# Kernel tuning notes

Measured on AMD Instinct MI355X. Metric: run time of the kernel, lower is better.

## Reference

```python
import math
import jax, jax.numpy as jnp
import numpy as np

B, C, DM, H = 4, 2048, 128, 8  # batch, after_reduced_cnn_size (seq), d_model, heads
DPH = DM // H                  # 16
K = 7                          # causal conv kernel size


def _causal_conv1d(x, w, b):
    # x: (B, C, L); w: (C_out, C_in, K); left-pad by K-1 -> causal, 'same' length
    xp = jnp.pad(x, ((0, 0), (0, 0), (w.shape[-1] - 1, 0)))
    y = jax.lax.conv_general_dilated(xp, w, (1,), 'VALID',
                                     dimension_numbers=('NCH', 'OIH', 'NCH'))
    return y + b[None, :, None]


def _split_heads(x):
    # (B, S, H*DPH) layout after view: (B, C, DM) -> (B, H, C, DPH)
    return x.reshape(x.shape[0], -1, H, DPH).transpose(0, 2, 1, 3)


def setup_inputs() -> dict:
    rng = jax.random.key(0)
    ks = jax.random.split(rng, 9)
    conv_scale = 1.0 / math.sqrt(C * K)
    lin_scale = 1.0 / math.sqrt(DM)
    return {
        'query': jax.random.normal(ks[0], (B, C, DM), dtype=jnp.float32),
        'key': jax.random.normal(ks[1], (B, C, DM), dtype=jnp.float32),
        'value': jax.random.normal(ks[2], (B, C, DM), dtype=jnp.float32),
        'conv_k_w': jax.random.normal(ks[3], (C, C, K), dtype=jnp.float32) * conv_scale,
        'conv_k_b': jnp.zeros((C,), dtype=jnp.float32),
        'conv_v_w': jax.random.normal(ks[4], (C, C, K), dtype=jnp.float32) * conv_scale,
        'conv_v_b': jnp.zeros((C,), dtype=jnp.float32),
        'lin_w': jax.random.normal(ks[5], (DM, DM), dtype=jnp.float32) * lin_scale,
        'lin_b': jnp.zeros((DM,), dtype=jnp.float32),
    }


def reference(query, key, value, conv_k_w, conv_k_b, conv_v_w, conv_v_b, lin_w, lin_b):
    # query used as-is; key/value pass through causal convs (convs[1], convs[2])
    q = _split_heads(query)                                   # (B,H,C,DPH)
    k = _split_heads(_causal_conv1d(key, conv_k_w, conv_k_b))  # (B,H,C,DPH)
    v = _split_heads(_causal_conv1d(value, conv_v_w, conv_v_b))
    scores = jnp.einsum('bhqd,bhkd->bhqk', q, k) / math.sqrt(DPH)
    p = jax.nn.softmax(scores, axis=-1)                       # (B,H,C,C)
    x = jnp.einsum('bhqk,bhkd->bhqd', p, v)                   # dropout p=0 => same as x_raw
    x = x.transpose(0, 2, 1, 3).reshape(x.shape[0], -1, H * DPH)
    return x @ lin_w.T + lin_b
```

## Files before the change

### kernel.cpp

```cpp
#include <hip/hip_runtime.h>
#include <cstdint>
#include <cstddef>

#define B_   4
#define C_   2048
#define DM_  128
#define H_   8
#define KK_  14336
#define N_   512

#define KSPLIT 8
#define KPB   1792
#define NITER 56

typedef unsigned short u16;
typedef __attribute__((ext_vector_type(8))) short  s16x8;
typedef __attribute__((ext_vector_type(4))) float  f32x4;

typedef const __attribute__((address_space(1))) void gvoid;
typedef __attribute__((address_space(3))) void lvoid;

__device__ __forceinline__ void gl2lds16(const void* g, void* l) {
    __builtin_amdgcn_global_load_lds((gvoid*)g, (lvoid*)l, 16, 0, 0);
}

__device__ __forceinline__ u16 f2bf(float f) {
    uint32_t u = __builtin_bit_cast(uint32_t, f);
    u += 0x7fffu + ((u >> 16) & 1u);
    return (u16)(u >> 16);
}
__device__ __forceinline__ uint32_t pk2(float a, float b) {
    return (uint32_t)f2bf(a) | ((uint32_t)f2bf(b) << 16);
}

__global__ __launch_bounds__(256) void zero_f4(float4* __restrict__ p, int n4) {
    int i = blockIdx.x * 256 + threadIdx.x;
    if (i < n4) p[i] = make_float4(0.f, 0.f, 0.f, 0.f);
}

__global__ __launch_bounds__(256) void prep_bimt(const float* __restrict__ key,
                                                 const float* __restrict__ value,
                                                 u16* __restrict__ bk,
                                                 u16* __restrict__ bv) {
    const float* src = blockIdx.z ? value : key;
    u16*         dst = blockIdx.z ? bv : bk;
    int gid = blockIdx.x * 256 + threadIdx.x;
    int cp = gid & 1023;
    int n  = gid >> 10;
    int b = n >> 7, l = n & 127;
    const float* s0 = src + (size_t)(b * C_ + cp * 2) * DM_;
    u16 hh[14];
#pragma unroll
    for (int r = 0; r < 2; ++r) {
#pragma unroll
        for (int t = 0; t < 7; ++t) {
            int j = l + t - 6;
            float v = (j >= 0) ? s0[r * DM_ + j] : 0.0f;
            hh[r * 7 + t] = f2bf(v);
        }
    }
    uint32_t* D = (uint32_t*)dst + (size_t)n * (KK_ / 2) + cp * 7;
#pragma unroll
    for (int i = 0; i < 7; ++i)
        D[i] = (uint32_t)hh[2 * i] | ((uint32_t)hh[2 * i + 1] << 16);
}

__global__ __launch_bounds__(256) void prep_q(const float4* __restrict__ q, uint2* __restrict__ qb) {
    int i = blockIdx.x * 256 + threadIdx.x;
    float4 v = q[i];
    uint2 r;
    r.x = pk2(v.x * 0.25f, v.y * 0.25f);
    r.y = pk2(v.z * 0.25f, v.w * 0.25f);
    qb[i] = r;
}

__global__ __launch_bounds__(256, 2) void conv_gemm(
        const float* __restrict__ Wk, const float* __restrict__ Wv,
        const u16* __restrict__ Bk, const u16* __restrict__ Bv,
        float* __restrict__ Yk, float* __restrict__ Yv) {
    const int conv = blockIdx.z >> 3;
    const int sk   = blockIdx.z & 7;
    const float* W  = conv ? Wv : Wk;
    const u16*   Bm = conv ? Bv : Bk;
    float*       Y  = conv ? Yv : Yk;
    const int m0 = blockIdx.x * 128;
    const int n0 = blockIdx.y * 256;
    const int kbeg = sk * KPB;

    __shared__ __align__(16) u16 Al[2][128 * 32];
    __shared__ __align__(16) u16 Bl[2][256 * 32];

    const int tid = threadIdx.x;
    const int wave = tid >> 6, lane = tid & 63;
    const int l16 = lane & 15, quad = lane >> 4;
    const int wm = wave >> 1, wn = wave & 1;

    const int arow = tid >> 1, ahalf = tid & 1;
    const float* wp = W + (size_t)(m0 + arow) * KK_ + kbeg + ahalf * 16;
    const int asw = (arow >> 1) & 3;
    const int aoff0 = arow * 32 + (((ahalf * 2)     ^ asw) * 8);
    const int aoff1 = arow * 32 + (((ahalf * 2 + 1) ^ asw) * 8);

    const u16* bgp[4];
    int boff[4];
    {
        const int br = lane >> 2, bs = lane & 3;
#pragma unroll
        for (int p = 0; p < 4; ++p) {
            int row = wave * 64 + p * 16 + br;
            int gc = (bs ^ ((row >> 1) & 3)) * 8;
            bgp[p] = Bm + (size_t)(n0 + row) * KK_ + kbeg + gc;
            boff[p] = (wave * 64 + p * 16) * 32;
        }
    }

    f32x4 acc[4][8];
#pragma unroll
    for (int i = 0; i < 4; ++i)
#pragma unroll
        for (int j = 0; j < 8; ++j) acc[i][j] = (f32x4){0.f, 0.f, 0.f, 0.f};

    float4 wr0, wr1, wr2, wr3;
    {
        float4 a0 = *(const float4*)(wp);
        float4 a1 = *(const float4*)(wp + 4);
        float4 a2 = *(const float4*)(wp + 8);
        float4 a3 = *(const float4*)(wp + 12);
        uint4 p0, p1;
        p0.x = pk2(a0.x, a0.y); p0.y = pk2(a0.z, a0.w);
        p0.z = pk2(a1.x, a1.y); p0.w = pk2(a1.z, a1.w);
        p1.x = pk2(a2.x, a2.y); p1.y = pk2(a2.z, a2.w);
        p1.z = pk2(a3.x, a3.y); p1.w = pk2(a3.z, a3.w);
        *(uint4*)&Al[0][aoff0] = p0;
        *(uint4*)&Al[0][aoff1] = p1;
#pragma unroll
        for (int p = 0; p < 4; ++p)
            gl2lds16(bgp[p], &Bl[0][boff[p]]);
        wr0 = *(const float4*)(wp + 32);
        wr1 = *(const float4*)(wp + 36);
        wr2 = *(const float4*)(wp + 40);
        wr3 = *(const float4*)(wp + 44);
    }

    int c = 0;
    for (int ks = 0; ks < NITER; ++ks) {
        __syncthreads();
        s16x8 af[4];
#pragma unroll
        for (int fm = 0; fm < 4; ++fm) {
            int r = wm * 64 + fm * 16 + l16;
            af[fm] = *(const s16x8*)&Al[c][r * 32 + ((quad ^ ((r >> 1) & 3)) * 8)];
        }
        s16x8 bfr[4];
#pragma unroll
        for (int fn = 0; fn < 4; ++fn) {
            int n = wn * 128 + fn * 16 + l16;
            bfr[fn] = *(const s16x8*)&Bl[c][n * 32 + ((quad ^ ((n >> 1) & 3)) * 8)];
        }
        const int kn  = (ks + 1 < NITER) ? ks + 1 : ks;
        const int kn2 = (ks + 2 < NITER) ? ks + 2 : 0;
#pragma unroll
        for (int p = 0; p < 4; ++p)
            gl2lds16(bgp[p] + (size_t)kn * 32, &Bl[c ^ 1][boff[p]]);
        {
            uint4 p0, p1;
            p0.x = pk2(wr0.x, wr0.y); p0.y = pk2(wr0.z, wr0.w);
            p0.z = pk2(wr1.x, wr1.y); p0.w = pk2(wr1.z, wr1.w);
            p1.x = pk2(wr2.x, wr2.y); p1.y = pk2(wr2.z, wr2.w);
            p1.z = pk2(wr3.x, wr3.y); p1.w = pk2(wr3.z, wr3.w);
            *(uint4*)&Al[c ^ 1][aoff0] = p0;
            *(uint4*)&Al[c ^ 1][aoff1] = p1;
        }
        wr0 = *(const float4*)(wp + (size_t)kn2 * 32);
        wr1 = *(const float4*)(wp + (size_t)kn2 * 32 + 4);
        wr2 = *(const float4*)(wp + (size_t)kn2 * 32 + 8);
        wr3 = *(const float4*)(wp + (size_t)kn2 * 32 + 12);
#pragma unroll
        for (int fm = 0; fm < 4; ++fm)
#pragma unroll
            for (int fn = 0; fn < 4; ++fn)
                acc[fm][fn] = __builtin_amdgcn_mfma_f32_16x16x32_bf16(af[fm], bfr[fn], acc[fm][fn], 0, 0, 0);
#pragma unroll
        for (int fn = 0; fn < 4; ++fn) {
            int n = wn * 128 + (fn + 4) * 16 + l16;
            bfr[fn] = *(const s16x8*)&Bl[c][n * 32 + ((quad ^ ((n >> 1) & 3)) * 8)];
        }
#pragma unroll
        for (int fm = 0; fm < 4; ++fm)
#pragma unroll
            for (int fn = 0; fn < 4; ++fn)
                acc[fm][fn + 4] = __builtin_amdgcn_mfma_f32_16x16x32_bf16(af[fm], bfr[fn], acc[fm][fn + 4], 0, 0, 0);
        c ^= 1;
    }

#pragma unroll
    for (int fm = 0; fm < 4; ++fm) {
        int m = m0 + wm * 64 + fm * 16 + quad * 4;
#pragma unroll
        for (int fn = 0; fn < 8; ++fn) {
            int n = n0 + wn * 128 + fn * 16 + l16;
            int bb = n >> 7, ll = n & 127;
            float* yp = Y + ((size_t)(bb * C_ + m)) * DM_ + ll;
#pragma unroll
            for (int r = 0; r < 4; ++r)
                atomicAdd(yp + (size_t)r * DM_, acc[fm][fn][r]);
        }
    }
}

__global__ __launch_bounds__(256) void kv_prep(
        const float* __restrict__ Yk, const float* __restrict__ Yv,
        const float* __restrict__ bkb, const float* __restrict__ bvb,
        u16* __restrict__ Kbf, u16* __restrict__ Vbf) {
    int gid = blockIdx.x * 256 + threadIdx.x;
    int key = gid & 2047;
    int bh  = gid >> 11;
    int b = bh >> 3, h = bh & 7;
    size_t src = ((size_t)(b * C_ + key)) * DM_ + h * 16;
    float kb = bkb[key], vb = bvb[key];

    float4 k0 = *(const float4*)(Yk + src);
    float4 k1 = *(const float4*)(Yk + src + 4);
    float4 k2 = *(const float4*)(Yk + src + 8);
    float4 k3 = *(const float4*)(Yk + src + 12);
    uint4 pA, pB;
    pA.x = pk2(k0.x + kb, k0.y + kb); pA.y = pk2(k0.z + kb, k0.w + kb);
    pA.z = pk2(k1.x + kb, k1.y + kb); pA.w = pk2(k1.z + kb, k1.w + kb);
    pB.x = pk2(k2.x + kb, k2.y + kb); pB.y = pk2(k2.z + kb, k2.w + kb);
    pB.z = pk2(k3.x + kb, k3.y + kb); pB.w = pk2(k3.z + kb, k3.w + kb);
    u16* kd = Kbf + ((size_t)bh * C_ + key) * 16;
    *(uint4*)kd       = pA;
    *(uint4*)(kd + 8) = pB;

    float4 v0 = *(const float4*)(Yv + src);
    float4 v1 = *(const float4*)(Yv + src + 4);
    float4 v2 = *(const float4*)(Yv + src + 8);
    float4 v3 = *(const float4*)(Yv + src + 12);
    float vf[16] = {v0.x, v0.y, v0.z, v0.w, v1.x, v1.y, v1.z, v1.w,
                    v2.x, v2.y, v2.z, v2.w, v3.x, v3.y, v3.z, v3.w};
    u16* vdst = Vbf + (size_t)bh * 16 * C_ + key;
#pragma unroll
    for (int d = 0; d < 16; ++d)
        vdst[(size_t)d * C_] = f2bf(vf[d] + vb);
}

__global__ __launch_bounds__(256, 4) void attn_k(
        const u16* __restrict__ Kbf, const u16* __restrict__ Vbf,
        const u16* __restrict__ qb, u16* __restrict__ att) {
    const int q0 = blockIdx.x * 64;
    const int bh = blockIdx.y;
    const int b = bh >> 3, h = bh & 7;

    __shared__ __align__(16) u16 Kl[128 * 24];
    __shared__ __align__(16) u16 Vl[16 * 128];
    __shared__ __align__(16) u16 Pl[64 * 136];

    const int tid = threadIdx.x;
    const int wave = tid >> 6, lane = tid & 63;
    const int l16 = lane & 15, quad = lane >> 4;
    const float LOG2E = 1.44269504088896340736f;

    const u16* kgp = Kbf + ((size_t)bh * C_ + (tid >> 1)) * 16 + (tid & 1) * 8;
    u16* kld = &Kl[(tid >> 1) * 24 + (tid & 1) * 8];
    const int vd = wave * 4 + (lane >> 4);
    const u16* vgp = Vbf + ((size_t)bh * 16 + vd) * C_ + (size_t)(((lane & 15) ^ (vd & 7)) * 8);
    u16* vld = &Vl[wave * 4 * 128];

    s16x8 qf = {};
    if (quad < 2) {
        const u16* qp = qb + ((size_t)(b * C_ + q0 + wave * 16 + l16)) * DM_ + h * 16 + quad * 8;
        qf = *(const s16x8*)qp;
    }
    f32x4 o = (f32x4){0.f, 0.f, 0.f, 0.f};
    float mr[4] = {-3e38f, -3e38f, -3e38f, -3e38f};
    float lr[4] = {0.f, 0.f, 0.f, 0.f};

    for (int kt = 0; kt < 16; ++kt) {
        const int k0 = kt * 128;
        __syncthreads();
        {
            uint4 kv = *(const uint4*)(kgp + (size_t)k0 * 16);
            *(uint4*)kld = kv;
            gl2lds16(vgp + k0, vld);
        }
        __syncthreads();

        f32x4 sf[8];
#pragma unroll
        for (int fn = 0; fn < 8; ++fn) {
            s16x8 kb = {};
            if (quad < 2) kb = *(const s16x8*)&Kl[(fn * 16 + l16) * 24 + quad * 8];
            sf[fn] = __builtin_amdgcn_mfma_f32_16x16x32_bf16(qf, kb, (f32x4){0.f, 0.f, 0.f, 0.f}, 0, 0, 0);
        }

        float mt[4];
#pragma unroll
        for (int r = 0; r < 4; ++r) {
            float m = sf[0][r];
#pragma unroll
            for (int fn = 1; fn < 8; ++fn) m = fmaxf(m, sf[fn][r]);
            m = fmaxf(m, __shfl_xor(m, 1));
            m = fmaxf(m, __shfl_xor(m, 2));
            m = fmaxf(m, __shfl_xor(m, 4));
            m = fmaxf(m, __shfl_xor(m, 8));
            mt[r] = m;
        }
        float al[4], ps[4];
#pragma unroll
        for (int r = 0; r < 4; ++r) {
            float mnew = fmaxf(mr[r], mt[r]);
            al[r] = exp2f((mr[r] - mnew) * LOG2E);
            mr[r] = mnew;
            ps[r] = 0.f;
        }
#pragma unroll
        for (int fn = 0; fn < 8; ++fn) {
#pragma unroll
            for (int r = 0; r < 4; ++r) {
                float p = exp2f((sf[fn][r] - mr[r]) * LOG2E);
                ps[r] += p;
                Pl[(wave * 16 + quad * 4 + r) * 136 + fn * 16 + l16] = f2bf(p);
            }
        }
#pragma unroll
        for (int r = 0; r < 4; ++r) {
            float t = ps[r];
            t += __shfl_xor(t, 1);
            t += __shfl_xor(t, 2);
            t += __shfl_xor(t, 4);
            t += __shfl_xor(t, 8);
            lr[r] = lr[r] * al[r] + t;
            o[r] *= al[r];
        }
#pragma unroll
        for (int ko = 0; ko < 4; ++ko) {
            s16x8 pa = *(const s16x8*)&Pl[(wave * 16 + l16) * 136 + ko * 32 + quad * 8];
            s16x8 vb = *(const s16x8*)&Vl[l16 * 128 + (((ko * 4 + quad) ^ (l16 & 7)) * 8)];
            o = __builtin_amdgcn_mfma_f32_16x16x32_bf16(pa, vb, o, 0, 0, 0);
        }
    }

#pragma unroll
    for (int r = 0; r < 4; ++r) {
        float inv = 1.0f / lr[r];
        int row = q0 + wave * 16 + quad * 4 + r;
        att[((size_t)(b * C_ + row)) * DM_ + h * 16 + l16] = f2bf(o[r] * inv);
    }
}

__global__ __launch_bounds__(256, 2) void lin_k(
        const u16* __restrict__ att, const float* __restrict__ lw,
        const float* __restrict__ lb, float* __restrict__ out) {
    const int r0 = blockIdx.x * 32;
    __shared__ __align__(16) u16 Wl[128 * 136];
    __shared__ __align__(16) u16 Atl[32 * 136];
    const int tid = threadIdx.x;
    const int wave = tid >> 6, lane = tid & 63;
    const int l16 = lane & 15, quad = lane >> 4;

    {
        int j = tid >> 1, half = tid & 1;
        const float* src = lw + (size_t)j * DM_ + half * 64;
        u16* dstp = &Wl[j * 136 + half * 64];
#pragma unroll
        for (int c = 0; c < 8; ++c) {
            float4 f0 = *(const float4*)(src + c * 8);
            float4 f1 = *(const float4*)(src + c * 8 + 4);
            uint4 p;
            p.x = pk2(f0.x, f0.y); p.y = pk2(f0.z, f0.w);
            p.z = pk2(f1.x, f1.y); p.w = pk2(f1.z, f1.w);
            *(uint4*)(dstp + c * 8) = p;
        }
    }
    {
        int row = tid >> 3, seg = tid & 7;
        const uint4* src = (const uint4*)(att + ((size_t)(r0 + row)) * DM_ + seg * 16);
        uint4 a0 = src[0], a1 = src[1];
        *(uint4*)&Atl[row * 136 + seg * 16]     = a0;
        *(uint4*)&Atl[row * 136 + seg * 16 + 8] = a1;
    }
    __syncthreads();

    const int wn0 = wave * 32;
    f32x4 acc[2][2];
#pragma unroll
    for (int i = 0; i < 2; ++i)
#pragma unroll
        for (int j = 0; j < 2; ++j) acc[i][j] = (f32x4){0.f, 0.f, 0.f, 0.f};
#pragma unroll
    for (int ko = 0; ko < 4; ++ko) {
        s16x8 af[2], bf[2];
#pragma unroll
        for (int fm = 0; fm < 2; ++fm)
            af[fm] = *(const s16x8*)&Atl[(fm * 16 + l16) * 136 + ko * 32 + quad * 8];
#pragma unroll
        for (int fn = 0; fn < 2; ++fn)
            bf[fn] = *(const s16x8*)&Wl[(wn0 + fn * 16 + l16) * 136 + ko * 32 + quad * 8];
#pragma unroll
        for (int fm = 0; fm < 2; ++fm)
#pragma unroll
            for (int fn = 0; fn < 2; ++fn)
                acc[fm][fn] = __builtin_amdgcn_mfma_f32_16x16x32_bf16(af[fm], bf[fn], acc[fm][fn], 0, 0, 0);
    }
#pragma unroll
    for (int fm = 0; fm < 2; ++fm) {
#pragma unroll
        for (int fn = 0; fn < 2; ++fn) {
            int col = wn0 + fn * 16 + l16;
            float bias = lb[col];
#pragma unroll
            for (int r = 0; r < 4; ++r) {
                int row = r0 + fm * 16 + quad * 4 + r;
                out[(size_t)row * DM_ + col] = acc[fm][fn][r] + bias;
            }
        }
    }
}

extern "C" void kernel_launch(void* const* d_in, const int* in_sizes, int n_in,
                              void* d_out, int out_size, void* d_ws, size_t ws_size,
                              hipStream_t stream) {
    const float* query = (const float*)d_in[0];
    const float* key   = (const float*)d_in[1];
    const float* value = (const float*)d_in[2];
    const float* wk    = (const float*)d_in[3];
    const float* bk    = (const float*)d_in[4];
    const float* wv    = (const float*)d_in[5];
    const float* bv    = (const float*)d_in[6];
    const float* lw    = (const float*)d_in[7];
    const float* lb    = (const float*)d_in[8];
    float* out = (float*)d_out;

    char* ws = (char*)d_ws;
    u16*   bimt_k = (u16*)(ws);
    u16*   bimt_v = (u16*)(ws + 14680064);
    float* yk     = (float*)(ws + 29360128);
    float* yv     = (float*)(ws + 33554432);
    u16*   qbf    = (u16*)(ws + 37748736);
    u16*   att    = (u16*)(ws + 39845888);
    u16*   kbf    = (u16*)(ws + 41943040);
    u16*   vbf    = (u16*)(ws + 44040192);

    zero_f4<<<2048, 256, 0, stream>>>((float4*)yk, 524288);
    prep_bimt<<<dim3(2048, 1, 2), 256, 0, stream>>>(key, value, bimt_k, bimt_v);
    prep_q<<<1024, 256, 0, stream>>>((const float4*)query, (uint2*)qbf);
    conv_gemm<<<dim3(16, 2, 16), 256, 0, stream>>>(wk, wv, bimt_k, bimt_v, yk, yv);
    kv_prep<<<256, 256, 0, stream>>>(yk, yv, bk, bv, kbf, vbf);
    attn_k<<<dim3(32, 32), 256, 0, stream>>>(kbf, vbf, qbf, att);
    lin_k<<<256, 256, 0, stream>>>(att, lw, lb, out);
}
```

Measured before the change: 482.5 us.

## Triple-buffer B tile and use explicit vmcnt waits in conv GEMM pipeline

Turns the conv GEMM main loop into a three-stage pipeline for the B operand in LDS and a two-stage register prefetch for the fp32 weights. Inline-asm global loads and explicit s_waitcnt vmcnt/lgkmcnt counts replace the compiler-managed waits, and a single barrier at the end of each iteration replaces the one at the top. The goal is to keep more global loads in flight while the MFMAs run, so the kernel stalls less on memory latency. The extra B buffer raises LDS per block, which may cut occupancy. The hand-counted waits also depend on how many loads are actually outstanding, so a wrong count would be a correctness risk.

After: 482.2 us. No clear change (-0.1%).

```diff
diff --git a/kernel.cpp b/kernel.cpp
--- a/kernel.cpp
+++ b/kernel.cpp
@@ -22,6 +22,10 @@
 
 __device__ __forceinline__ void gl2lds16(const void* g, void* l) {
     __builtin_amdgcn_global_load_lds((gvoid*)g, (lvoid*)l, 16, 0, 0);
+}
+
+__device__ __forceinline__ void gload4(float4& d, const float* p) {
+    asm volatile("global_load_dwordx4 %0, %1, off" : "=v"(d) : "v"(p) : "memory");
 }
 
 __device__ __forceinline__ u16 f2bf(float f) {
@@ -88,7 +92,7 @@
     const int kbeg = sk * KPB;
 
     __shared__ __align__(16) u16 Al[2][128 * 32];
-    __shared__ __align__(16) u16 Bl[2][256 * 32];
+    __shared__ __align__(16) u16 Bl[3][256 * 32];
 
     const int tid = threadIdx.x;
     const int wave = tid >> 6, lane = tid & 63;
@@ -122,10 +126,19 @@
 
     float4 wr0, wr1, wr2, wr3;
     {
-        float4 a0 = *(const float4*)(wp);
-        float4 a1 = *(const float4*)(wp + 4);
-        float4 a2 = *(const float4*)(wp + 8);
-        float4 a3 = *(const float4*)(wp + 12);
+#pragma unroll
+        for (int p = 0; p < 4; ++p)
+            gl2lds16(bgp[p], &Bl[0][boff[p]]);
+        float4 a0, a1, a2, a3;
+        gload4(a0, wp);      gload4(a1, wp + 4);
+        gload4(a2, wp + 8);  gload4(a3, wp + 12);
+#pragma unroll
+        for (int p = 0; p < 4; ++p)
+            gl2lds16(bgp[p] + 32, &Bl[1][boff[p]]);
+        gload4(wr0, wp + 32); gload4(wr1, wp + 36);
+        gload4(wr2, wp + 40); gload4(wr3, wp + 44);
+        asm volatile("s_waitcnt vmcnt(8)" ::: "memory");
+        __builtin_amdgcn_sched_barrier(0);
         uint4 p0, p1;
         p0.x = pk2(a0.x, a0.y); p0.y = pk2(a0.z, a0.w);
         p0.z = pk2(a1.x, a1.y); p0.w = pk2(a1.z, a1.w);
@@ -133,48 +146,32 @@
         p1.z = pk2(a3.x, a3.y); p1.w = pk2(a3.z, a3.w);
         *(uint4*)&Al[0][aoff0] = p0;
         *(uint4*)&Al[0][aoff1] = p1;
-#pragma unroll
-        for (int p = 0; p < 4; ++p)
-            gl2lds16(bgp[p], &Bl[0][boff[p]]);
-        wr0 = *(const float4*)(wp + 32);
-        wr1 = *(const float4*)(wp + 36);
-        wr2 = *(const float4*)(wp + 40);
-        wr3 = *(const float4*)(wp + 44);
-    }
-
-    int c = 0;
-    for (int ks = 0; ks < NITER; ++ks) {
-        __syncthreads();
+        asm volatile("s_waitcnt lgkmcnt(0)" ::: "memory");
+        __builtin_amdgcn_sched_barrier(0);
+        __builtin_amdgcn_s_barrier();
+    }
+
+    int bcur = 0;
+    for (int t = 0; t < NITER; ++t) {
+        const int ap = t & 1;
+        int bst = bcur - 1; if (bst < 0) bst = 2;
+        const int kb = (t + 2 < NITER) ? t + 2 : NITER - 1;
+
         s16x8 af[4];
 #pragma unroll
         for (int fm = 0; fm < 4; ++fm) {
             int r = wm * 64 + fm * 16 + l16;
-            af[fm] = *(const s16x8*)&Al[c][r * 32 + ((quad ^ ((r >> 1) & 3)) * 8)];
+            af[fm] = *(const s16x8*)&Al[ap][r * 32 + ((quad ^ ((r >> 1) & 3)) * 8)];
         }
         s16x8 bfr[4];
 #pragma unroll
         for (int fn = 0; fn < 4; ++fn) {
             int n = wn * 128 + fn * 16 + l16;
-            bfr[fn] = *(const s16x8*)&Bl[c][n * 32 + ((quad ^ ((n >> 1) & 3)) * 8)];
-        }
-        const int kn  = (ks + 1 < NITER) ? ks + 1 : ks;
-        const int kn2 = (ks + 2 < NITER) ? ks + 2 : 0;
+            bfr[fn] = *(const s16x8*)&Bl[bcur][n * 32 + ((quad ^ ((n >> 1) & 3)) * 8)];
+        }
 #pragma unroll
         for (int p = 0; p < 4; ++p)
-            gl2lds16(bgp[p] + (size_t)kn * 32, &Bl[c ^ 1][boff[p]]);
-        {
-            uint4 p0, p1;
-            p0.x = pk2(wr0.x, wr0.y); p0.y = pk2(wr0.z, wr0.w);
-            p0.z = pk2(wr1.x, wr1.y); p0.w = pk2(wr1.z, wr1.w);
-            p1.x = pk2(wr2.x, wr2.y); p1.y = pk2(wr2.z, wr2.w);
-            p1.z = pk2(wr3.x, wr3.y); p1.w = pk2(wr3.z, wr3.w);
-            *(uint4*)&Al[c ^ 1][aoff0] = p0;
-            *(uint4*)&Al[c ^ 1][aoff1] = p1;
-        }
-        wr0 = *(const float4*)(wp + (size_t)kn2 * 32);
-        wr1 = *(const float4*)(wp + (size_t)kn2 * 32 + 4);
-        wr2 = *(const float4*)(wp + (size_t)kn2 * 32 + 8);
-        wr3 = *(const float4*)(wp + (size_t)kn2 * 32 + 12);
+            gl2lds16(bgp[p] + (size_t)kb * 32, &Bl[bst][boff[p]]);
 #pragma unroll
         for (int fm = 0; fm < 4; ++fm)
 #pragma unroll
@@ -183,15 +180,39 @@
 #pragma unroll
         for (int fn = 0; fn < 4; ++fn) {
             int n = wn * 128 + (fn + 4) * 16 + l16;
-            bfr[fn] = *(const s16x8*)&Bl[c][n * 32 + ((quad ^ ((n >> 1) & 3)) * 8)];
+            bfr[fn] = *(const s16x8*)&Bl[bcur][n * 32 + ((quad ^ ((n >> 1) & 3)) * 8)];
         }
 #pragma unroll
         for (int fm = 0; fm < 4; ++fm)
 #pragma unroll
             for (int fn = 0; fn < 4; ++fn)
                 acc[fm][fn + 4] = __builtin_amdgcn_mfma_f32_16x16x32_bf16(af[fm], bfr[fn], acc[fm][fn + 4], 0, 0, 0);
-        c ^= 1;
-    }
+
+        asm volatile("s_waitcnt vmcnt(4)" ::: "memory");
+        __builtin_amdgcn_sched_barrier(0);
+
+        {
+            uint4 q0, q1;
+            q0.x = pk2(wr0.x, wr0.y); q0.y = pk2(wr0.z, wr0.w);
+            q0.z = pk2(wr1.x, wr1.y); q0.w = pk2(wr1.z, wr1.w);
+            q1.x = pk2(wr2.x, wr2.y); q1.y = pk2(wr2.z, wr2.w);
+            q1.z = pk2(wr3.x, wr3.y); q1.w = pk2(wr3.z, wr3.w);
+            *(uint4*)&Al[ap ^ 1][aoff0] = q0;
+            *(uint4*)&Al[ap ^ 1][aoff1] = q1;
+        }
+        gload4(wr0, wp + (size_t)kb * 32);
+        gload4(wr1, wp + (size_t)kb * 32 + 4);
+        gload4(wr2, wp + (size_t)kb * 32 + 8);
+        gload4(wr3, wp + (size_t)kb * 32 + 12);
+
+        asm volatile("s_waitcnt lgkmcnt(0)" ::: "memory");
+        __builtin_amdgcn_sched_barrier(0);
+        __builtin_amdgcn_s_barrier();
+
+        bcur = (bcur == 2) ? 0 : bcur + 1;
+    }
+    asm volatile("s_waitcnt vmcnt(0)" ::: "memory");
+    __builtin_amdgcn_sched_barrier(0);
 
 #pragma unroll
     for (int fm = 0; fm < 4; ++fm) {
```
